# Optimization experiments

Measured on AMD Instinct MI355X. Metric: run time of the kernel, lower is better.

Reference implementation:

```python
import jax, jax.numpy as jnp
import numpy as np


def _avgpool(x, k):
    # x: (N, C, H, W), k divides H and W
    if k == 1:
        return x
    N, C, H, W = x.shape
    return x.reshape(N, C, H // k, k, W // k, k).mean(axis=(3, 5))


def _pairwise_sum(mu1, var1, mu2, var2):
    # mu*, var*: (N, D). Broadcast to (N, N, D), fused elementwise chain + full sum.
    d = mu1[:, None, :] - mu2[None, :, :]
    v = var1[:, None, :] + var2[None, :, :]
    return jnp.sum(jnp.exp(-0.5 * d * d / v) / jnp.sqrt(v))


def setup_inputs() -> dict:
    key = jax.random.key(0)
    k1, k2, k3, k4 = jax.random.split(key, 4)
    shape = (64, 16, 64, 64)
    return {
        "mu_a": jax.random.normal(k1, shape, dtype=jnp.float32),
        "logvar_a": jax.random.normal(k2, shape, dtype=jnp.float32),
        "mu_b": jax.random.normal(k3, shape, dtype=jnp.float32),
        "logvar_b": jax.random.normal(k4, shape, dtype=jnp.float32),
        "kern": 2,
    }


def reference(mu_a, logvar_a, mu_b, logvar_b, kern):
    k2 = float(kern * kern)
    mu_a_p = _avgpool(mu_a, kern)
    mu_b_p = _avgpool(mu_b, kern)
    var_a = _avgpool(jnp.exp(logvar_a), kern) / k2
    var_b = _avgpool(jnp.exp(logvar_b), kern) / k2

    N = mu_a_p.shape[0]
    mu_a_f = mu_a_p.reshape(N, -1)
    mu_b_f = mu_b_p.reshape(N, -1)
    var_a_f = var_a.reshape(N, -1)
    var_b_f = var_b.reshape(N, -1)

    vaa = _pairwise_sum(mu_a_f, var_a_f, mu_a_f, var_a_f)
    vab = _pairwise_sum(mu_a_f, var_a_f, mu_b_f, var_b_f)
    vbb = _pairwise_sum(mu_b_f, var_b_f, mu_b_f, var_b_f)
    return vaa + vbb - 2.0 * vab
```

## Files before the change

### kernel.cpp

```cpp
#include <hip/hip_runtime.h>

#define N_ 64
#define C_ 16
#define H_ 64
#define W_ 64

#define TRI_TILES 72
#define TILES 272
#define DCHUNKS 16
#define PAIR_BLOCKS (TILES * DCHUNKS)

#define TWO_LN2   1.3862943611198906f
#define SQRT_2LN2 1.1774100225154747f


__global__ __launch_bounds__(256) void pool_kernel(
    const float* __restrict__ mu_a, const float* __restrict__ lv_a,
    const float* __restrict__ mu_b, const float* __restrict__ lv_b,
    const int* __restrict__ kern_p, float* __restrict__ ws) {
    const int k = kern_p[0];
    const float LOG2E = 1.44269504088896f;

    if (k == 2) {
        const int Np = (N_ * C_ * H_ * W_) >> 2;
        const int Q  = Np >> 2;
        const int total = 4 * Q;
        for (int g = blockIdx.x * blockDim.x + threadIdx.x; g < total;
             g += gridDim.x * blockDim.x) {
            const int a  = g >> 18;
            const int r4 = g & (Q - 1);
            const int pw4 = (r4 & 7) << 2;
            const int t   = r4 >> 3;
            const int ph  = t & 31;
            const int nc  = t >> 5;
            const float* src = (a == 0) ? mu_a : (a == 1) ? lv_a : (a == 2) ? mu_b : lv_b;
            const bool is_var = (a & 1);
            const float* p0 = src + nc * (H_ * W_) + (ph * 2) * W_ + pw4 * 2;
            float4 r0a = *(const float4*)(p0);
            float4 r0b = *(const float4*)(p0 + 4);
            float4 r1a = *(const float4*)(p0 + W_);
            float4 r1b = *(const float4*)(p0 + W_ + 4);
            float o0, o1, o2, o3;
            if (is_var) {
#define E_(x) __builtin_amdgcn_exp2f((x) * LOG2E)
                o0 = E_(r0a.x) + E_(r0a.y) + E_(r1a.x) + E_(r1a.y);
                o1 = E_(r0a.z) + E_(r0a.w) + E_(r1a.z) + E_(r1a.w);
                o2 = E_(r0b.x) + E_(r0b.y) + E_(r1b.x) + E_(r1b.y);
                o3 = E_(r0b.z) + E_(r0b.w) + E_(r1b.z) + E_(r1b.w);
#undef E_
                const float s = (1.0f / 16.0f) * TWO_LN2;
                o0 *= s; o1 *= s; o2 *= s; o3 *= s;
            } else {
                o0 = r0a.x + r0a.y + r1a.x + r1a.y;
                o1 = r0a.z + r0a.w + r1a.z + r1a.w;
                o2 = r0b.x + r0b.y + r1b.x + r1b.y;
                o3 = r0b.z + r0b.w + r1b.z + r1b.w;
                const float s = 0.25f;
                o0 *= s; o1 *= s; o2 *= s; o3 *= s;
            }
            *(float4*)(ws + (size_t)a * Np + (size_t)r4 * 4) = make_float4(o0, o1, o2, o3);
        }
    } else {
        const int Hp = H_ / k, Wp = W_ / k;
        const int Np = N_ * C_ * Hp * Wp;
        const float inv_k2 = 1.0f / (float)(k * k);
        const float inv_k4 = inv_k2 * inv_k2 * TWO_LN2;
        const int total = 4 * Np;
        for (int p = blockIdx.x * blockDim.x + threadIdx.x; p < total;
             p += gridDim.x * blockDim.x) {
            const int a  = p / Np;
            const int r  = p - a * Np;
            const int pw = r % Wp;
            const int t1 = r / Wp;
            const int ph = t1 % Hp;
            const int nc = t1 / Hp;
            const float* src = (a == 0) ? mu_a : (a == 1) ? lv_a : (a == 2) ? mu_b : lv_b;
            const bool is_var = (a & 1);
            const int base = nc * (H_ * W_) + (ph * k) * W_ + (pw * k);
            float s = 0.0f;
            for (int dy = 0; dy < k; ++dy) {
                const float* row = src + base + dy * W_;
                for (int dx = 0; dx < k; ++dx) {
                    float x = row[dx];
                    s += is_var ? __builtin_amdgcn_exp2f(x * LOG2E) : x;
                }
            }
            ws[(size_t)a * Np + r] = s * (is_var ? inv_k4 : inv_k2);
        }
    }
}

__global__ __launch_bounds__(256) void pair_kernel(float* __restrict__ ws,
                                                   const int* __restrict__ kern_p) {
    const int k = kern_p[0];
    const int D  = C_ * (H_ / k) * (W_ / k);
    const int Np = N_ * D;

    const float* mu_a = ws;
    const float* va   = ws + (size_t)Np;
    const float* mu_b = ws + (size_t)2 * Np;
    const float* vb   = ws + (size_t)3 * Np;
    float* partials   = ws + (size_t)4 * Np;

    const int c = blockIdx.x & (DCHUNKS - 1);
    const int t = blockIdx.x >> 4;
    int set, it, jt;
    if (t >= 2 * TRI_TILES) {
        set = 2;
        const int tt = t - 2 * TRI_TILES;
        it = tt >> 3;
        jt = tt & 7;
    } else {
        set = (t >= TRI_TILES) ? 1 : 0;
        const int tt = set ? (t - TRI_TILES) : t;
        int g = 0, cum = 0;
        while (cum + (g >> 1) + 1 <= tt) { cum += (g >> 1) + 1; ++g; }
        it = g;
        jt = tt - cum;
    }
    const int i0 = it * 4, j0 = jt * 8;

    const float *mu1, *v1, *mu2, *v2;
    if (set == 0)      { mu1 = mu2 = mu_a; v1 = v2 = va; }
    else if (set == 1) { mu1 = mu2 = mu_b; v1 = v2 = vb; }
    else               { mu1 = mu_a; v1 = va; mu2 = mu_b; v2 = vb; }

    const bool uniform = (set == 2) || (jt < (it >> 1));
    const float wU = (set == 2) ? -2.0f : 2.0f;

#define TERM(acc, mx1, sx1, mx2, sx2)                                  \
    {                                                                  \
        float v  = (sx1) + (sx2);                                      \
        float rs = __builtin_amdgcn_rsqf(v);                           \
        float d  = (mx1) - (mx2);                                      \
        float t_ = d * rs;                                             \
        float e  = __builtin_amdgcn_exp2f(-(t_ * t_));                 \
        acc = fmaf(e, rs, acc);                                        \
    }
#define TERMW(acc, mx1, sx1, mx2, sx2, w)                              \
    {                                                                  \
        float v  = (sx1) + (sx2);                                      \
        float rs = __builtin_amdgcn_rsqf(v);                           \
        float d  = (mx1) - (mx2);                                      \
        float t_ = d * rs;                                             \
        float e  = __builtin_amdgcn_exp2f(-(t_ * t_));                 \
        acc = fmaf((w), e * rs, acc);                                  \
    }

    float acc[4][4];
    #pragma unroll
    for (int ir = 0; ir < 4; ++ir)
        #pragma unroll
        for (int q = 0; q < 4; ++q) acc[ir][q] = 0.0f;

    float wmul = 1.0f;

    if (D == 16384) {
        const int base = (c << 10) + ((int)threadIdx.x << 2);
        const float* pim = mu1 + (size_t)i0 * 16384 + base;
        const float* piv = v1  + (size_t)i0 * 16384 + base;
        const float* pjm = mu2 + (size_t)j0 * 16384 + base;
        const float* pjv = v2  + (size_t)j0 * 16384 + base;
        float4 im[4], iv[4];
        #pragma unroll
        for (int ir = 0; ir < 4; ++ir) {
            im[ir] = *(const float4*)(pim + (size_t)ir * 16384);
            iv[ir] = *(const float4*)(piv + (size_t)ir * 16384);
        }
        float4 jm = *(const float4*)(pjm);
        float4 jv = *(const float4*)(pjv);
        if (uniform) {
            wmul = wU;
            #pragma unroll
            for (int j8 = 0; j8 < 8; ++j8) {
                float4 nm, nv;
                if (j8 < 7) {
                    nm = *(const float4*)(pjm + (size_t)(j8 + 1) * 16384);
                    nv = *(const float4*)(pjv + (size_t)(j8 + 1) * 16384);
                }
                #pragma unroll
                for (int ir = 0; ir < 4; ++ir) {
                    TERM(acc[ir][0], im[ir].x, iv[ir].x, jm.x, jv.x)
                    TERM(acc[ir][1], im[ir].y, iv[ir].y, jm.y, jv.y)
                    TERM(acc[ir][2], im[ir].z, iv[ir].z, jm.z, jv.z)
                    TERM(acc[ir][3], im[ir].w, iv[ir].w, jm.w, jv.w)
                }
                if (j8 < 7) { jm = nm; jv = nv; }
            }
        } else {
            #pragma unroll
            for (int j8 = 0; j8 < 8; ++j8) {
                float4 nm, nv;
                if (j8 < 7) {
                    nm = *(const float4*)(pjm + (size_t)(j8 + 1) * 16384);
                    nv = *(const float4*)(pjv + (size_t)(j8 + 1) * 16384);
                }
                const int jj = j0 + j8;
                #pragma unroll
                for (int ir = 0; ir < 4; ++ir) {
                    const int ii = i0 + ir;
                    const float w = (jj > ii) ? 0.0f : (jj == ii) ? 1.0f : 2.0f;
                    TERMW(acc[ir][0], im[ir].x, iv[ir].x, jm.x, jv.x, w)
                    TERMW(acc[ir][1], im[ir].y, iv[ir].y, jm.y, jv.y, w)
                    TERMW(acc[ir][2], im[ir].z, iv[ir].z, jm.z, jv.z, w)
                    TERMW(acc[ir][3], im[ir].w, iv[ir].w, jm.w, jv.w, w)
                }
                if (j8 < 7) { jm = nm; jv = nv; }
            }
        }
    } else {
        const int cs = D / DCHUNKS;
        const int lo = c * cs, hi = lo + cs;
        for (int e = lo + (int)threadIdx.x; e < hi; e += 256) {
            #pragma unroll
            for (int j8 = 0; j8 < 8; ++j8) {
                const int jj = j0 + j8;
                const float mj = mu2[(size_t)jj * D + e];
                const float vj = v2 [(size_t)jj * D + e];
                #pragma unroll
                for (int ir = 0; ir < 4; ++ir) {
                    const int ii = i0 + ir;
                    const float w = (set == 2) ? -2.0f
                                  : (jj > ii) ? 0.0f : (jj == ii) ? 1.0f : 2.0f;
                    const float mi = mu1[(size_t)ii * D + e];
                    const float vi = v1 [(size_t)ii * D + e];
                    TERMW(acc[ir][j8 & 3], mi, vi, mj, vj, w)
                }
            }
        }
    }
#undef TERM
#undef TERMW

    float tot = 0.0f;
    #pragma unroll
    for (int ir = 0; ir < 4; ++ir)
        #pragma unroll
        for (int q = 0; q < 4; ++q) tot += acc[ir][q];
    tot *= wmul * SQRT_2LN2;

    for (int off = 32; off > 0; off >>= 1)
        tot += __shfl_down(tot, off, 64);
    __shared__ float wsum[4];
    const int lane = threadIdx.x & 63;
    const int wid  = threadIdx.x >> 6;
    if (lane == 0) wsum[wid] = tot;
    __syncthreads();
    if (threadIdx.x == 0) {
        partials[blockIdx.x] = wsum[0] + wsum[1] + wsum[2] + wsum[3];
    }
}

__global__ __launch_bounds__(256) void reduce_kernel(const float* __restrict__ ws,
                                                     const int* __restrict__ kern_p,
                                                     float* __restrict__ out) {
    const int k = kern_p[0];
    const int D  = C_ * (H_ / k) * (W_ / k);
    const int Np = N_ * D;
    const float* partials = ws + (size_t)4 * Np;

    float s = 0.0f;
    for (int p = threadIdx.x; p < PAIR_BLOCKS; p += 256) s += partials[p];
    for (int off = 32; off > 0; off >>= 1)
        s += __shfl_down(s, off, 64);
    __shared__ float wsum[4];
    const int lane = threadIdx.x & 63;
    const int wid  = threadIdx.x >> 6;
    if (lane == 0) wsum[wid] = s;
    __syncthreads();
    if (threadIdx.x == 0) out[0] = wsum[0] + wsum[1] + wsum[2] + wsum[3];
}

extern "C" void kernel_launch(void* const* d_in, const int* in_sizes, int n_in,
                              void* d_out, int out_size, void* d_ws, size_t ws_size,
                              hipStream_t stream) {
    const float* mu_a = (const float*)d_in[0];
    const float* lv_a = (const float*)d_in[1];
    const float* mu_b = (const float*)d_in[2];
    const float* lv_b = (const float*)d_in[3];
    const int*   kern = (const int*)d_in[4];
    float* out = (float*)d_out;
    float* ws  = (float*)d_ws;

    pool_kernel<<<4096, 256, 0, stream>>>(mu_a, lv_a, mu_b, lv_b, kern, ws);
    pair_kernel<<<PAIR_BLOCKS, 256, 0, stream>>>(ws, kern);
    reduce_kernel<<<1, 256, 0, stream>>>(ws, kern, out);
}
```

Measured before the change: 147.1 us.

## Use square 8x8 pair tiles with compile-time triangular masking on diagonal

Changes the pairwise tile from 4x8 rows to 8x8, halving the number of tiles and blocks and doubling the row reuse of each loaded j vector. Diagonal tiles now skip upper-triangle work with compile-time branches instead of computing terms weighted by zero, so no wasted exp/rsq work is done. The cost is more registers (32 accumulators plus 16 float4 row values), which may lower occupancy, and the explicit prefetch of the next j row is dropped. Fewer blocks (2176) may also reduce load balance.

```diff
diff --git a/kernel.cpp b/kernel.cpp
--- a/kernel.cpp
+++ b/kernel.cpp
@@ -5,8 +5,8 @@
 #define H_ 64
 #define W_ 64
 
-#define TRI_TILES 72
-#define TILES 272
+#define TRI_TILES 36
+#define TILES 136
 #define DCHUNKS 16
 #define PAIR_BLOCKS (TILES * DCHUNKS)
 
@@ -114,19 +114,19 @@
         set = (t >= TRI_TILES) ? 1 : 0;
         const int tt = set ? (t - TRI_TILES) : t;
         int g = 0, cum = 0;
-        while (cum + (g >> 1) + 1 <= tt) { cum += (g >> 1) + 1; ++g; }
+        while (cum + g + 1 <= tt) { cum += g + 1; ++g; }
         it = g;
         jt = tt - cum;
     }
-    const int i0 = it * 4, j0 = jt * 8;
+    const int i0 = it * 8, j0 = jt * 8;
 
     const float *mu1, *v1, *mu2, *v2;
     if (set == 0)      { mu1 = mu2 = mu_a; v1 = v2 = va; }
     else if (set == 1) { mu1 = mu2 = mu_b; v1 = v2 = vb; }
     else               { mu1 = mu_a; v1 = va; mu2 = mu_b; v2 = vb; }
 
-    const bool uniform = (set == 2) || (jt < (it >> 1));
-    const float wU = (set == 2) ? -2.0f : 2.0f;
+    const bool diag = (set < 2) && (it == jt);
+    const float wU  = (set == 2) ? -2.0f : 2.0f;
 
 #define TERM(acc, mx1, sx1, mx2, sx2)                                  \
     {                                                                  \
@@ -147,9 +147,9 @@
         acc = fmaf((w), e * rs, acc);                                  \
     }
 
-    float acc[4][4];
+    float acc[8][4];
     #pragma unroll
-    for (int ir = 0; ir < 4; ++ir)
+    for (int ir = 0; ir < 8; ++ir)
         #pragma unroll
         for (int q = 0; q < 4; ++q) acc[ir][q] = 0.0f;
 
@@ -157,55 +157,46 @@
 
     if (D == 16384) {
         const int base = (c << 10) + ((int)threadIdx.x << 2);
-        const float* pim = mu1 + (size_t)i0 * 16384 + base;
-        const float* piv = v1  + (size_t)i0 * 16384 + base;
-        const float* pjm = mu2 + (size_t)j0 * 16384 + base;
-        const float* pjv = v2  + (size_t)j0 * 16384 + base;
-        float4 im[4], iv[4];
+        float4 im[8], iv[8];
         #pragma unroll
-        for (int ir = 0; ir < 4; ++ir) {
-            im[ir] = *(const float4*)(pim + (size_t)ir * 16384);
-            iv[ir] = *(const float4*)(piv + (size_t)ir * 16384);
-        }
-        float4 jm = *(const float4*)(pjm);
-        float4 jv = *(const float4*)(pjv);
-        if (uniform) {
+        for (int ir = 0; ir < 8; ++ir) {
+            im[ir] = *(const float4*)(mu1 + (size_t)(i0 + ir) * 16384 + base);
+            iv[ir] = *(const float4*)(v1  + (size_t)(i0 + ir) * 16384 + base);
+        }
+        if (!diag) {
             wmul = wU;
             #pragma unroll
             for (int j8 = 0; j8 < 8; ++j8) {
-                float4 nm, nv;
-                if (j8 < 7) {
-                    nm = *(const float4*)(pjm + (size_t)(j8 + 1) * 16384);
-                    nv = *(const float4*)(pjv + (size_t)(j8 + 1) * 16384);
-                }
+                const float4 jm = *(const float4*)(mu2 + (size_t)(j0 + j8) * 16384 + base);
+                const float4 jv = *(const float4*)(v2  + (size_t)(j0 + j8) * 16384 + base);
                 #pragma unroll
-                for (int ir = 0; ir < 4; ++ir) {
+                for (int ir = 0; ir < 8; ++ir) {
                     TERM(acc[ir][0], im[ir].x, iv[ir].x, jm.x, jv.x)
                     TERM(acc[ir][1], im[ir].y, iv[ir].y, jm.y, jv.y)
                     TERM(acc[ir][2], im[ir].z, iv[ir].z, jm.z, jv.z)
                     TERM(acc[ir][3], im[ir].w, iv[ir].w, jm.w, jv.w)
                 }
-                if (j8 < 7) { jm = nm; jv = nv; }
             }
         } else {
             #pragma unroll
             for (int j8 = 0; j8 < 8; ++j8) {
-                float4 nm, nv;
-                if (j8 < 7) {
-                    nm = *(const float4*)(pjm + (size_t)(j8 + 1) * 16384);
-                    nv = *(const float4*)(pjv + (size_t)(j8 + 1) * 16384);
-                }
-                const int jj = j0 + j8;
+                const float4 jm = *(const float4*)(mu2 + (size_t)(j0 + j8) * 16384 + base);
+                const float4 jv = *(const float4*)(v2  + (size_t)(j0 + j8) * 16384 + base);
                 #pragma unroll
-                for (int ir = 0; ir < 4; ++ir) {
-                    const int ii = i0 + ir;
-                    const float w = (jj > ii) ? 0.0f : (jj == ii) ? 1.0f : 2.0f;
-                    TERMW(acc[ir][0], im[ir].x, iv[ir].x, jm.x, jv.x, w)
-                    TERMW(acc[ir][1], im[ir].y, iv[ir].y, jm.y, jv.y, w)
-                    TERMW(acc[ir][2], im[ir].z, iv[ir].z, jm.z, jv.z, w)
-                    TERMW(acc[ir][3], im[ir].w, iv[ir].w, jm.w, jv.w, w)
-                }
-                if (j8 < 7) { jm = nm; jv = nv; }
+                for (int ir = 0; ir < 8; ++ir) {
+                    if (ir < j8) continue;
+                    if (ir == j8) {
+                        TERM(acc[ir][0], im[ir].x, iv[ir].x, jm.x, jv.x)
+                        TERM(acc[ir][1], im[ir].y, iv[ir].y, jm.y, jv.y)
+                        TERM(acc[ir][2], im[ir].z, iv[ir].z, jm.z, jv.z)
+                        TERM(acc[ir][3], im[ir].w, iv[ir].w, jm.w, jv.w)
+                    } else {
+                        TERMW(acc[ir][0], im[ir].x, iv[ir].x, jm.x, jv.x, 2.0f)
+                        TERMW(acc[ir][1], im[ir].y, iv[ir].y, jm.y, jv.y, 2.0f)
+                        TERMW(acc[ir][2], im[ir].z, iv[ir].z, jm.z, jv.z, 2.0f)
+                        TERMW(acc[ir][3], im[ir].w, iv[ir].w, jm.w, jv.w, 2.0f)
+                    }
+                }
             }
         }
     } else {
@@ -218,7 +209,7 @@
                 const float mj = mu2[(size_t)jj * D + e];
                 const float vj = v2 [(size_t)jj * D + e];
                 #pragma unroll
-                for (int ir = 0; ir < 4; ++ir) {
+                for (int ir = 0; ir < 8; ++ir) {
                     const int ii = i0 + ir;
                     const float w = (set == 2) ? -2.0f
                                   : (jj > ii) ? 0.0f : (jj == ii) ? 1.0f : 2.0f;
@@ -234,7 +225,7 @@
 
     float tot = 0.0f;
     #pragma unroll
-    for (int ir = 0; ir < 4; ++ir)
+    for (int ir = 0; ir < 8; ++ir)
         #pragma unroll
         for (int q = 0; q < 4; ++q) tot += acc[ir][q];
     tot *= wmul * SQRT_2LN2;
```

Measured after the change: 151.4 us. +2.9%, slower.
